# Optimization experiments

Measured on AMD Instinct MI355X. Metric: run time of the kernel, lower is better.

## Reference

```python
import jax, jax.numpy as jnp
import numpy as np

N, E, B, H, F = 20000, 400000, 200, 10, 78
HID = H * F  # 780
SEQ, VOC, EMB, NF, KS = 1000, 26, 128, 32, 8
CONV_OUT = SEQ - KS + 1  # 993


def setup_inputs() -> dict:
    key = jax.random.key(0)
    ks = jax.random.split(key, 40)
    g = lambda i, shape, s=0.05: jax.random.normal(ks[i], shape, jnp.float32) * s
    inp = {
        "x": jax.random.normal(ks[0], (N, F), jnp.float32),
        "edge_index": jax.random.randint(ks[1], (2, E), 0, N),
        "batch": jnp.sort(jax.random.randint(ks[2], (N,), 0, B)),
        "target": jax.random.randint(ks[3], (B, SEQ), 0, VOC),
        # GATConv(78 -> 78, heads=10)
        "gat_W": g(4, (F, HID)),
        "gat_a_src": g(5, (H, F)),
        "gat_a_dst": g(6, (H, F)),
        "gat_b": g(7, (HID,)),
        # GCNConv(780 -> 780)
        "gcn_W": g(8, (HID, HID)),
        "gcn_b": g(9, (HID,)),
        # graph MLP head
        "fcg1_W": g(10, (HID, 1500)), "fcg1_b": g(11, (1500,)),
        "fcg2_W": g(12, (1500, 128)), "fcg2_b": g(13, (128,)),
        # protein branch
        "emb": g(14, (VOC, EMB)),
        "cW": g(15, (NF, EMB, KS)), "cb": g(16, (NF,)),
        "fxt_W": g(17, (NF * CONV_OUT, 128)), "fxt_b": g(18, (128,)),
        # fusion MLP
        "f1_W": g(19, (256, 1024)), "f1_b": g(20, (1024,)),
        "f2_W": g(21, (1024, 512)), "f2_b": g(22, (512,)),
        "f3_W": g(23, (512, 256)), "f3_b": g(24, (256,)),
        "f4_W": g(25, (256, 128)), "f4_b": g(26, (128,)),
        "o_W": g(27, (128, 1)), "o_b": g(28, (1,)),
    }
    return inp


def _graph_branch(x, edge_index, batch, gat_W, gat_a_src, gat_a_dst, gat_b,
                  gcn_W, gcn_b, fcg1_W, fcg1_b, fcg2_W, fcg2_b):
    n = x.shape[0]
    loops = jnp.arange(n)
    src = jnp.concatenate([edge_index[0], loops])  # add self loops (PyG default)
    dst = jnp.concatenate([edge_index[1], loops])
    # --- GATConv ---
    h = (x @ gat_W).reshape(n, H, F)  # [N,H,F]
    a_s = jnp.einsum("nhf,hf->nh", h, gat_a_src)
    a_d = jnp.einsum("nhf,hf->nh", h, gat_a_dst)
    e = jax.nn.leaky_relu(a_s[src] + a_d[dst], 0.2)  # [Etot,H]
    m = jax.ops.segment_max(e, dst, num_segments=n)
    ex = jnp.exp(e - m[dst])
    den = jax.ops.segment_sum(ex, dst, num_segments=n)
    alpha = ex / den[dst]
    agg = jax.ops.segment_sum(h[src] * alpha[:, :, None], dst, num_segments=n)
    x1 = jax.nn.relu(agg.reshape(n, HID) + gat_b)
    # --- GCNConv (sym norm with self loops) ---
    deg = jax.ops.segment_sum(jnp.ones_like(dst, jnp.float32), dst, num_segments=n)
    dinv = jax.lax.rsqrt(jnp.maximum(deg, 1.0))
    norm = dinv[src] * dinv[dst]
    h2 = x1 @ gcn_W
    x2 = jax.ops.segment_sum(h2[src] * norm[:, None], dst, num_segments=n) + gcn_b
    x2 = jax.nn.relu(x2)
    # --- global add pool + MLP ---
    xg = jax.ops.segment_sum(x2, batch, num_segments=B)
    xg = jax.nn.relu(xg @ fcg1_W + fcg1_b)  # dropout = identity (eval)
    return xg @ fcg2_W + fcg2_b


def _protein_branch(target, emb, cW, cb, fxt_W, fxt_b):
    et = emb[target]  # [B,SEQ,EMB]
    c = jax.lax.conv_general_dilated(
        et.transpose(0, 2, 1), cW, (1,), "VALID",
        dimension_numbers=("NCH", "OIH", "NCH"))  # [B,NF,993]
    c = c + cb[None, :, None]
    return c.reshape(c.shape[0], NF * CONV_OUT) @ fxt_W + fxt_b


def reference(x, edge_index, batch, target, gat_W, gat_a_src, gat_a_dst, gat_b,
              gcn_W, gcn_b, fcg1_W, fcg1_b, fcg2_W, fcg2_b, emb, cW, cb,
              fxt_W, fxt_b, f1_W, f1_b, f2_W, f2_b, f3_W, f3_b, f4_W, f4_b,
              o_W, o_b):
    xg = _graph_branch(x, edge_index, batch, gat_W, gat_a_src, gat_a_dst, gat_b,
                       gcn_W, gcn_b, fcg1_W, fcg1_b, fcg2_W, fcg2_b)
    xt = _protein_branch(target, emb, cW, cb, fxt_W, fxt_b)
    xc = jnp.concatenate([xg, xt], axis=1)  # [B,256]
    xc = jax.nn.relu(xc @ f1_W + f1_b)
    xc = jax.nn.relu(xc @ f2_W + f2_b)
    xc = jax.nn.relu(xc @ f3_W + f3_b)
    xc = jax.nn.relu(xc @ f4_W + f4_b)
    return xc @ o_W + o_b  # [B,1]
```

## Files before the change

### kernel.cpp

```cpp
#include <hip/hip_runtime.h>
#include <hip/hip_bf16.h>
#include <math.h>

typedef __hip_bfloat16 bf16;
typedef __attribute__((ext_vector_type(8))) short short8v;
typedef __attribute__((ext_vector_type(4))) float float4v;

#define NODES 20000
#define EDG   400000
#define ETOT  (EDG + NODES)
#define GB    200
#define HEADS 10
#define FD    78
#define HIDD  780
#define SEQL  1000
#define VOCS  26
#define EMBD  128
#define NFC   32
#define KSZ   8
#define COUT  993
#define KFXT  (NFC * COUT)

#define MPAD  20096
#define NPADB 896
#define KP2   800
#define HP    800
#define PNL   2
#define PF    400
#define MB2   208
#define FXT_KS 128
#define HK    96
#define AGS   960


__device__ __forceinline__ float us2f(unsigned short u) {
  unsigned int i = ((unsigned int)u) << 16; float f; __builtin_memcpy(&f, &i, 4); return f;
}
__device__ __forceinline__ float b2f(bf16 v) { return __bfloat162float(v); }
__device__ __forceinline__ float ldany(const void* p, size_t i, int m) {
  if (m) return ((const float*)p)[i];
  return b2f(((const bf16*)p)[i]);
}
__device__ __forceinline__ bool nanf_(float v) { return v != v; }
__device__ __forceinline__ unsigned short f2us(float v) {
  bf16 b = __float2bfloat16(v); unsigned short u; __builtin_memcpy(&u, &b, 2); return u;
}

__global__ void k_detect(const void* x, int* diag) {
  int t = threadIdx.x;
  const unsigned short* u = (const unsigned short*)x;
  int hit = 0;
  for (int i = t; i < 4096; i += 256) {
    float v = us2f(u[i]);
    if (nanf_(v) || fabsf(v) > 1e6f) hit = 1;
  }
  if (hit) diag[1] = 1;
}

__global__ void k_tr_gcnw(const void* gw, bf16* Wt, const int* diag) {
  int idx = blockIdx.x * 256 + threadIdx.x;
  if (idx >= NPADB * KP2) return;
  int mode = diag[1];
  int n = idx / KP2, k = idx % KP2;
  float v = (n < HIDD && k < HIDD) ? ldany(gw, (size_t)k * HIDD + n, mode) : 0.f;
  Wt[idx] = __float2bfloat16(v);
}

__global__ void k_prep_wt2(const void* gw, bf16* Wt2, const int* diag) {
  int idx = blockIdx.x * 256 + threadIdx.x;
  if (idx >= HEADS * 128 * HK) return;
  int mode = diag[1];
  int h = idx / (128 * HK);
  int r = idx % (128 * HK);
  int n = r / HK, k = r % HK;
  float v = (n < FD && k < FD) ? ldany(gw, (size_t)k * HIDD + h * FD + n, mode) : 0.f;
  Wt2[idx] = __float2bfloat16(v);
}

__global__ void k_zero_x1pad(bf16* x1p) {
  int i = blockIdx.x * 256 + threadIdx.x;
  int nr = (MPAD - NODES) * KP2;
  if (i < nr) {
    x1p[(size_t)NODES * KP2 + i] = __float2bfloat16(0.f);
  } else {
    int j = i - nr;
    if (j < NODES * 20) {
      int d = j / 20, c = HIDD + (j % 20);
      x1p[(size_t)d * KP2 + c] = __float2bfloat16(0.f);
    }
  }
}

#define MT 128
#define NT 128
#define BK 32
#define LP 40
__global__ __launch_bounds__(256) void k_gemm_mfma(const bf16* A, int lda,
                                                   const bf16* Bt, int ldb,
                                                   bf16* C, int ldc, int Ncap,
                                                   int M, int Kp) {
  __shared__ __align__(16) bf16 As[MT * LP];
  __shared__ __align__(16) bf16 Bs[NT * LP];
  int t = threadIdx.x;
  int lane = t & 63, w = t >> 6;
  int wr = (w >> 1) * 64, wc = (w & 1) * 64;
  int quad = lane >> 4, mr = lane & 15;
  int m0 = blockIdx.y * MT, n0 = blockIdx.x * NT;
  float4v acc[4][4];
#pragma unroll
  for (int i = 0; i < 4; ++i)
#pragma unroll
    for (int j = 0; j < 4; ++j) acc[i][j] = (float4v){0.f, 0.f, 0.f, 0.f};

  for (int kc = 0; kc < Kp; kc += BK) {
#pragma unroll
    for (int i = 0; i < 4; ++i) {
      int c = t + i * 256;
      int row = c >> 3, col = (c & 7) * 4;
      *(uint2*)&As[row * LP + col] =
          *(const uint2*)&A[(size_t)(m0 + row) * lda + kc + col];
      *(uint2*)&Bs[row * LP + col] =
          *(const uint2*)&Bt[(size_t)(n0 + row) * ldb + kc + col];
    }
    __syncthreads();
    short8v af[4], bfr[4];
#pragma unroll
    for (int i = 0; i < 4; ++i)
      af[i] = *(const short8v*)&As[(wr + i * 16 + mr) * LP + quad * 8];
#pragma unroll
    for (int j = 0; j < 4; ++j)
      bfr[j] = *(const short8v*)&Bs[(wc + j * 16 + mr) * LP + quad * 8];
#pragma unroll
    for (int i = 0; i < 4; ++i)
#pragma unroll
      for (int j = 0; j < 4; ++j)
        acc[i][j] = __builtin_amdgcn_mfma_f32_16x16x32_bf16(af[i], bfr[j], acc[i][j], 0, 0, 0);
    __syncthreads();
  }
#pragma unroll
  for (int i = 0; i < 4; ++i) {
    int gm0 = m0 + wr + i * 16 + quad * 4;
#pragma unroll
    for (int j = 0; j < 4; ++j) {
      int gn = n0 + wc + j * 16 + mr;
      if (gn >= Ncap) continue;
#pragma unroll
      for (int r = 0; r < 4; ++r) {
        int gm = gm0 + r;
        if (gm < M) C[(size_t)gm * ldc + gn] = __float2bfloat16(acc[i][j][r]);
      }
    }
  }
}

__global__ __launch_bounds__(256) void k_hgemm(const bf16* aggx, const bf16* Wt2,
                                               const void* gat_b, bf16* x1,
                                               const int* diag) {
  __shared__ __align__(16) bf16 As[MT * LP];
  __shared__ __align__(16) bf16 Bs[NT * LP];
  int t = threadIdx.x;
  int lane = t & 63, w = t >> 6;
  int wr = (w >> 1) * 64, wc = (w & 1) * 64;
  int quad = lane >> 4, mr = lane & 15;
  int m0 = blockIdx.x * MT, h = blockIdx.y;
  int mode = diag[1];
  const bf16* A = aggx + (size_t)h * HK;
  const bf16* Bt = Wt2 + (size_t)h * 128 * HK;
  float4v acc[4][4];
#pragma unroll
  for (int i = 0; i < 4; ++i)
#pragma unroll
    for (int j = 0; j < 4; ++j) acc[i][j] = (float4v){0.f, 0.f, 0.f, 0.f};

  for (int kc = 0; kc < HK; kc += BK) {
#pragma unroll
    for (int i = 0; i < 4; ++i) {
      int c = t + i * 256;
      int row = c >> 3, col = (c & 7) * 4;
      *(uint2*)&As[row * LP + col] =
          *(const uint2*)&A[(size_t)(m0 + row) * AGS + kc + col];
      *(uint2*)&Bs[row * LP + col] =
          *(const uint2*)&Bt[(size_t)row * HK + kc + col];
    }
    __syncthreads();
    short8v af[4], bfr[4];
#pragma unroll
    for (int i = 0; i < 4; ++i)
      af[i] = *(const short8v*)&As[(wr + i * 16 + mr) * LP + quad * 8];
#pragma unroll
    for (int j = 0; j < 4; ++j)
      bfr[j] = *(const short8v*)&Bs[(wc + j * 16 + mr) * LP + quad * 8];
#pragma unroll
    for (int i = 0; i < 4; ++i)
#pragma unroll
      for (int j = 0; j < 4; ++j)
        acc[i][j] = __builtin_amdgcn_mfma_f32_16x16x32_bf16(af[i], bfr[j], acc[i][j], 0, 0, 0);
    __syncthreads();
  }
#pragma unroll
  for (int i = 0; i < 4; ++i) {
    int gm0 = m0 + wr + i * 16 + quad * 4;
#pragma unroll
    for (int j = 0; j < 4; ++j) {
      int gn = wc + j * 16 + mr;
      if (gn >= FD) continue;
      float bs = ldany(gat_b, h * FD + gn, mode);
#pragma unroll
      for (int r = 0; r < 4; ++r) {
        int gm = gm0 + r;
        if (gm < NODES)
          x1[(size_t)gm * KP2 + h * FD + gn] =
              __float2bfloat16(fmaxf(acc[i][j][r] + bs, 0.f));
      }
    }
  }
}

#define MLP_NT 64
#define MLP_BK 32
#define MLP_MT 208
#define MLP_LP 40
__global__ __launch_bounds__(256) void k_mlp_mfma(const void* A, int lda, const void* Bw,
                                                  const void* bias, float* out, int ostride,
                                                  int ooff, int M, int Nn, int K,
                                                  int ksplit, int aRelu, int aBf16,
                                                  const int* diag) {
  __shared__ __align__(16) bf16 As[MLP_MT * MLP_LP];
  __shared__ __align__(16) bf16 Bs[MLP_NT * MLP_LP];
  int mode = diag[1];
  int t = threadIdx.x;
  int lane = t & 63, w = t >> 6;
  int quad = lane >> 4, mr = lane & 15;
  int n0 = blockIdx.x * MLP_NT;
  int kz = blockIdx.y;
  int nchunks = (K + MLP_BK - 1) / MLP_BK;
  int cpk = (nchunks + ksplit - 1) / ksplit;
  int c0 = kz * cpk, c1 = c0 + cpk;
  if (c1 > nchunks) c1 = nchunks;
  float4v acc[13];
#pragma unroll
  for (int i = 0; i < 13; ++i) acc[i] = (float4v){0.f, 0.f, 0.f, 0.f};

  for (int c = c0; c < c1; ++c) {
    int k0 = c * MLP_BK;
    if (aBf16) {
      const bf16* Ab = (const bf16*)A;
      for (int e = t; e < MLP_MT * 4; e += 256) {
        int row = e >> 2, c8 = (e & 3) * 8;
        int gk = k0 + c8;
        if (row < M && gk + 7 < K) {
          *(uint4*)&As[row * MLP_LP + c8] = *(const uint4*)&Ab[(size_t)row * lda + gk];
        } else {
#pragma unroll
          for (int kk = 0; kk < 8; ++kk) {
            float v = (row < M && gk + kk < K) ? b2f(Ab[(size_t)row * lda + gk + kk]) : 0.f;
            As[row * MLP_LP + c8 + kk] = __float2bfloat16(v);
          }
        }
      }
    } else {
      const float* Af = (const float*)A;
      for (int e = t; e < MLP_MT * 8; e += 256) {
        int row = e >> 3, c4 = (e & 7) * 4;
        int gk = k0 + c4;
        float4 v4 = {0.f, 0.f, 0.f, 0.f};
        if (row < M) {
          if (gk + 3 < K) {
            v4 = *(const float4*)&Af[(size_t)row * lda + gk];
          } else {
            v4.x = (gk + 0 < K) ? Af[(size_t)row * lda + gk + 0] : 0.f;
            v4.y = (gk + 1 < K) ? Af[(size_t)row * lda + gk + 1] : 0.f;
            v4.z = (gk + 2 < K) ? Af[(size_t)row * lda + gk + 2] : 0.f;
            v4.w = (gk + 3 < K) ? Af[(size_t)row * lda + gk + 3] : 0.f;
          }
        }
        if (aRelu) {
          v4.x = fmaxf(v4.x, 0.f); v4.y = fmaxf(v4.y, 0.f);
          v4.z = fmaxf(v4.z, 0.f); v4.w = fmaxf(v4.w, 0.f);
        }
        bf16* dst = &As[row * MLP_LP + c4];
        dst[0] = __float2bfloat16(v4.x); dst[1] = __float2bfloat16(v4.y);
        dst[2] = __float2bfloat16(v4.z); dst[3] = __float2bfloat16(v4.w);
      }
    }
    for (int e = t; e < MLP_NT * MLP_BK; e += 256) {
      int k = e >> 6, col = e & 63;
      int gk = k0 + k, gn = n0 + col;
      float v = (gn < Nn && gk < K) ? ldany(Bw, (size_t)gk * Nn + gn, mode) : 0.f;
      Bs[col * MLP_LP + k] = __float2bfloat16(v);
    }
    __syncthreads();
    short8v bf = *(const short8v*)&Bs[(w * 16 + mr) * MLP_LP + quad * 8];
#pragma unroll
    for (int i = 0; i < 13; ++i) {
      short8v af = *(const short8v*)&As[(i * 16 + mr) * MLP_LP + quad * 8];
      acc[i] = __builtin_amdgcn_mfma_f32_16x16x32_bf16(af, bf, acc[i], 0, 0, 0);
    }
    __syncthreads();
  }
  int gn = n0 + w * 16 + mr;
  if (gn >= Nn) return;
  float bs = (kz == 0) ? ldany(bias, gn, mode) : 0.f;
#pragma unroll
  for (int i = 0; i < 13; ++i) {
    int gm0 = i * 16 + quad * 4;
#pragma unroll
    for (int r = 0; r < 4; ++r) {
      int gm = gm0 + r;
      if (gm >= M) break;
      float v = acc[i][r] + bs;
      float* op = &out[(size_t)gm * ostride + ooff + gn];
      if (ksplit == 1) *op = v;
      else atomicAdd(op, v);
    }
  }
}

__global__ __launch_bounds__(256) void k_fxt(const bf16* cT, const void* Bw,
                                             float* part, const int* diag) {
  __shared__ __align__(16) bf16 As[MLP_MT * MLP_LP];
  __shared__ __align__(16) bf16 Bs[MLP_NT * MLP_LP];
  int mode = diag[1];
  int t = threadIdx.x;
  int lane = t & 63, w = t >> 6;
  int quad = lane >> 4, mr = lane & 15;
  int n0 = blockIdx.x * MLP_NT;
  int kz = blockIdx.y;
  int nchunks = KFXT / MLP_BK;
  int cpk = (nchunks + FXT_KS - 1) / FXT_KS;
  int c0 = kz * cpk, c1 = c0 + cpk;
  if (c1 > nchunks) c1 = nchunks;
  float4v acc[13];
#pragma unroll
  for (int i = 0; i < 13; ++i) acc[i] = (float4v){0.f, 0.f, 0.f, 0.f};

  for (int c = c0; c < c1; ++c) {
    int k0 = c * MLP_BK;
    for (int e = t; e < 32 * 52; e += 256) {
      int kk = e / 52, bq = e % 52;
      uint2 u = *(const uint2*)&cT[(size_t)(k0 + kk) * MB2 + bq * 4];
      unsigned short* ap = (unsigned short*)As;
      int mb = bq * 4;
      ap[(mb + 0) * MLP_LP + kk] = (unsigned short)(u.x & 0xffffu);
      ap[(mb + 1) * MLP_LP + kk] = (unsigned short)(u.x >> 16);
      ap[(mb + 2) * MLP_LP + kk] = (unsigned short)(u.y & 0xffffu);
      ap[(mb + 3) * MLP_LP + kk] = (unsigned short)(u.y >> 16);
    }
    for (int e = t; e < MLP_NT * MLP_BK; e += 256) {
      int k = e >> 6, col = e & 63;
      float v = ldany(Bw, (size_t)(k0 + k) * 128 + (n0 + col), mode);
      Bs[col * MLP_LP + k] = __float2bfloat16(v);
    }
    __syncthreads();
    short8v bf = *(const short8v*)&Bs[(w * 16 + mr) * MLP_LP + quad * 8];
#pragma unroll
    for (int i = 0; i < 13; ++i) {
      short8v af = *(const short8v*)&As[(i * 16 + mr) * MLP_LP + quad * 8];
      acc[i] = __builtin_amdgcn_mfma_f32_16x16x32_bf16(af, bf, acc[i], 0, 0, 0);
    }
    __syncthreads();
  }
  int gnl = n0 + w * 16 + mr;
#pragma unroll
  for (int i = 0; i < 13; ++i) {
#pragma unroll
    for (int r = 0; r < 4; ++r) {
      int gm = i * 16 + quad * 4 + r;
      part[((size_t)kz * MB2 + gm) * 128 + gnl] = acc[i][r];
    }
  }
}

__global__ __launch_bounds__(128) void k_fxt_red(const float* part, const void* bias,
                                                 float* xc, const int* diag) {
  int gm = blockIdx.x, n = threadIdx.x;
  int mode = diag[1];
  float s = 0.f;
  for (int kz = 0; kz < FXT_KS; ++kz)
    s += part[((size_t)kz * MB2 + gm) * 128 + n];
  xc[(size_t)gm * 256 + 128 + n] = s + ldany(bias, n, mode);
}

__global__ void k_prep_ws(const void* gat_W, const void* a_src, const void* a_dst,
                          float* Ws, float* Wd, const int* diag) {
  int idx = blockIdx.x * 256 + threadIdx.x;
  if (idx >= FD * HEADS) return;
  int mode = diag[1];
  int k = idx / HEADS, hd = idx % HEADS;
  float s = 0.f, d = 0.f;
  for (int f = 0; f < FD; ++f) {
    float w = ldany(gat_W, (size_t)k * HIDD + hd * FD + f, mode);
    s += w * ldany(a_src, (size_t)hd * FD + f, mode);
    d += w * ldany(a_dst, (size_t)hd * FD + f, mode);
  }
  Ws[k * HEADS + hd] = s;
  Wd[k * HEADS + hd] = d;
}

__global__ void k_prep_mtab(const void* emb, const void* cW, float* Mtab, const int* diag) {
  int idx = blockIdx.x * 256 + threadIdx.x;
  if (idx >= NFC * KSZ * VOCS) return;
  int mode = diag[1];
  int o = idx / (KSZ * VOCS);
  int r = idx % (KSZ * VOCS);
  int k = r / VOCS, v = r % VOCS;
  float acc = 0.f;
  for (int i = 0; i < EMBD; ++i)
    acc += ldany(emb, (size_t)v * EMBD + i, mode) * ldany(cW, ((size_t)o * EMBD + i) * KSZ + k, mode);
  Mtab[idx] = acc;
}

__global__ __launch_bounds__(256) void k_asd(const void* x, const float* Ws, const float* Wd,
                                             float* a_s, float* a_d, const int* diag) {
  __shared__ unsigned short xs[256 * FD];
  __shared__ float ws_sh[FD * HEADS], wd_sh[FD * HEADS];
  int mode = diag[1];
  int nb = blockIdx.x * 256, t = threadIdx.x;
  for (int e = t; e < FD * HEADS; e += 256) { ws_sh[e] = Ws[e]; wd_sh[e] = Wd[e]; }
  for (int e = t; e < 256 * FD; e += 256) {
    int r = e / FD, c = e % FD;
    int gn = nb + r;
    float xv = (gn < NODES) ? ldany(x, (size_t)gn * FD + c, mode) : 0.f;
    xs[e] = f2us(xv);
  }
  __syncthreads();
  int n = nb + t;
  if (n >= NODES) return;
  float as[HEADS], ad[HEADS];
#pragma unroll
  for (int hd = 0; hd < HEADS; ++hd) { as[hd] = 0.f; ad[hd] = 0.f; }
  for (int f = 0; f < FD; ++f) {
    float xv = us2f(xs[t * FD + f]);
#pragma unroll
    for (int hd = 0; hd < HEADS; ++hd) {
      as[hd] += xv * ws_sh[f * HEADS + hd];
      ad[hd] += xv * wd_sh[f * HEADS + hd];
    }
  }
#pragma unroll
  for (int hd = 0; hd < HEADS; ++hd) {
    a_s[n * HEADS + hd] = as[hd];
    a_d[n * HEADS + hd] = ad[hd];
  }
}

__global__ void k_count(const int* ei, int* cnt, int* diag) {
  int e = blockIdx.x * 256 + threadIdx.x;
  if (e >= ETOT) return;
  int d = (e < EDG) ? ei[EDG + e] : (e - EDG);
  if ((unsigned)d >= NODES) { atomicOr(diag, 8192); d = 0; }
  atomicAdd(&cnt[d], 1);
}

__global__ __launch_bounds__(1024) void k_scan(const int* cnt, int* rowstart) {
  __shared__ int wsum[16];
  __shared__ int carry;
  int t = threadIdx.x;
  int lane = t & 63, wid = t >> 6;
  if (t == 0) carry = 0;
  __syncthreads();
  for (int c = 0; c < (NODES + 1023) / 1024; ++c) {
    int i = c * 1024 + t;
    int orig = (i < NODES) ? cnt[i] : 0;
    int v = orig;
#pragma unroll
    for (int off = 1; off < 64; off <<= 1) {
      int u = __shfl_up(v, off, 64);
      if (lane >= off) v += u;
    }
    if (lane == 63) wsum[wid] = v;
    __syncthreads();
    if (t == 0) {
      int s = carry;
      for (int j = 0; j < 16; ++j) { int tmp = wsum[j]; wsum[j] = s; s += tmp; }
      carry = s;
    }
    __syncthreads();
    if (i < NODES) rowstart[i] = v - orig + wsum[wid];
    __syncthreads();
  }
  if (t == 0) rowstart[NODES] = carry;
}

__global__ void k_dinv(const int* cnt, float* dinv) {
  int n = blockIdx.x * 256 + threadIdx.x;
  if (n >= NODES) return;
  int d = cnt[n];
  dinv[n] = rsqrtf((float)(d > 0 ? d : 1));
}

__global__ void k_scatter(const int* ei, const int* rowstart, int* cur, int* es_src,
                          int* diag) {
  int e = blockIdx.x * 256 + threadIdx.x;
  if (e >= ETOT) return;
  int s, d;
  if (e < EDG) { s = ei[e]; d = ei[EDG + e]; } else { s = e - EDG; d = s; }
  if ((unsigned)d >= NODES) { atomicOr(diag, 8192); d = 0; }
  if ((unsigned)s >= NODES) { atomicOr(diag, 8192); s = 0; }
  int pos = rowstart[d] + atomicAdd(&cur[d], 1);
  if ((unsigned)pos < (unsigned)ETOT) es_src[pos] = s;
  else atomicOr(diag, 1);
}

__global__ void k_csrchk(const int* cnt, const int* cur, const int* rowst, int* diag) {
  int n = blockIdx.x * 256 + threadIdx.x;
  if (n < NODES && cur[n] != cnt[n]) atomicOr(diag, 1);
  if (n == 0 && rowst[NODES] != ETOT) atomicOr(diag, 1);
}

__global__ void k_bseg(const int* batch, int* bstart, int* diag) {
  int i = blockIdx.x * 256 + threadIdx.x;
  if (i >= NODES) return;
  int bi = batch[i];
  if ((unsigned)bi >= GB) { atomicOr(diag, 8192); bi = GB - 1; }
  int bp;
  if (i == 0) bp = -1;
  else {
    bp = batch[i - 1];
    if ((unsigned)bp >= GB) bp = GB - 1;
  }
  for (int b = bp + 1; b <= bi; ++b) bstart[b] = i;
  if (i == NODES - 1)
    for (int b = bi + 1; b <= GB; ++b) bstart[b] = NODES;
}

__global__ __launch_bounds__(64) void k_alpha(const int* es_src, const int* rowst,
                                              const float* a_s, const float* a_d,
                                              float* alpha, int* diag) {
  int d = blockIdx.x, lane = threadIdx.x;
  int start = rowst[d], end = rowst[d + 1];
  float ad[HEADS];
#pragma unroll
  for (int j = 0; j < HEADS; ++j) ad[j] = a_d[d * HEADS + j];
  float mx[HEADS];
#pragma unroll
  for (int j = 0; j < HEADS; ++j) mx[j] = -INFINITY;
  for (int base = start; base < end; base += 64) {
    int ce = base + lane;
    if (ce < end) {
      int s = es_src[ce];
      if ((unsigned)s >= NODES) { atomicOr(diag, 1); s = 0; }
#pragma unroll
      for (int j = 0; j < HEADS; ++j) {
        float v = a_s[s * HEADS + j] + ad[j];
        v = v > 0.f ? v : 0.2f * v;
        mx[j] = fmaxf(mx[j], v);
      }
    }
  }
#pragma unroll
  for (int j = 0; j < HEADS; ++j)
    for (int off = 1; off < 64; off <<= 1) mx[j] = fmaxf(mx[j], __shfl_xor(mx[j], off, 64));
  float den[HEADS];
#pragma unroll
  for (int j = 0; j < HEADS; ++j) den[j] = 0.f;
  for (int base = start; base < end; base += 64) {
    int ce = base + lane;
    if (ce < end) {
      int s = es_src[ce];
      if ((unsigned)s >= NODES) s = 0;
#pragma unroll
      for (int j = 0; j < HEADS; ++j) {
        float v = a_s[s * HEADS + j] + ad[j];
        v = v > 0.f ? v : 0.2f * v;
        den[j] += expf(v - mx[j]);
      }
    }
  }
#pragma unroll
  for (int j = 0; j < HEADS; ++j)
    for (int off = 1; off < 64; off <<= 1) den[j] += __shfl_xor(den[j], off, 64);
  if (lane == 0 && (nanf_(den[0]) || nanf_(den[HEADS - 1]))) atomicOr(diag, 2);
  for (int base = start; base < end; base += 64) {
    int ce = base + lane;
    if (ce < end) {
      int s = es_src[ce];
      if ((unsigned)s >= NODES) s = 0;
#pragma unroll
      for (int j = 0; j < HEADS; ++j) {
        float v = a_s[s * HEADS + j] + ad[j];
        v = v > 0.f ? v : 0.2f * v;
        alpha[(size_t)ce * HEADS + j] = expf(v - mx[j]) / den[j];
      }
    }
  }
}

__global__ __launch_bounds__(64) void k_gatx(const int* es_src, const int* rowst,
                                             const float* alpha, const void* x,
                                             bf16* aggx, int* diag) {
  __shared__ int ssc[64];
  __shared__ float alw[64 * HEADS];
  int d = blockIdx.x, lane = threadIdx.x;
  int mode = diag[1];
  int start = rowst[d], end = rowst[d + 1];
  int f0 = 2 * lane;
  float acc[HEADS][2];
#pragma unroll
  for (int j = 0; j < HEADS; ++j) { acc[j][0] = 0.f; acc[j][1] = 0.f; }
  for (int base = start; base < end; base += 64) {
    int ce = base + lane;
    if (ce < end) {
      int s = es_src[ce];
      if ((unsigned)s >= NODES) { atomicOr(diag, 1); s = 0; }
      ssc[lane] = s;
#pragma unroll
      for (int j = 0; j < HEADS; ++j) alw[lane * HEADS + j] = alpha[(size_t)ce * HEADS + j];
    }
    __syncthreads();
    int cnt2 = end - base; if (cnt2 > 64) cnt2 = 64;
    if (lane < 39) {
      for (int e = 0; e < cnt2; ++e) {
        int ss = ssc[e];
        float xv0, xv1;
        if (mode) {
          const float* xf = (const float*)x;
          xv0 = xf[(size_t)ss * FD + f0];
          xv1 = xf[(size_t)ss * FD + f0 + 1];
        } else {
          unsigned int u = *(const unsigned int*)((const unsigned short*)x +
                                                  (size_t)ss * FD + f0);
          xv0 = us2f((unsigned short)(u & 0xffffu));
          xv1 = us2f((unsigned short)(u >> 16));
        }
        const float* al = &alw[e * HEADS];
#pragma unroll
        for (int j = 0; j < HEADS; ++j) {
          acc[j][0] += al[j] * xv0;
          acc[j][1] += al[j] * xv1;
        }
      }
    }
    __syncthreads();
  }
  if (lane < 48) {
    if (lane < 39 && (nanf_(acc[0][0]) || nanf_(acc[HEADS - 1][1]))) atomicOr(diag, 8);
    size_t rb = (size_t)d * AGS;
#pragma unroll
    for (int h = 0; h < HEADS; ++h) {
      unsigned short o0 = (f0 < FD) ? f2us(acc[h][0]) : (unsigned short)0;
      unsigned short o1 = (f0 + 1 < FD) ? f2us(acc[h][1]) : (unsigned short)0;
      unsigned int pack = (unsigned int)o0 | ((unsigned int)o1 << 16);
      *(unsigned int*)(aggx + rb + h * HK + f0) = pack;
    }
  }
}

__global__ __launch_bounds__(64) void k_gcng(const int* es_src, const int* rowst,
                                             const float* dinv, const bf16* h2,
                                             const void* gcn_b, bf16* x2b, int* diag) {
  __shared__ int ssc[64];
  __shared__ float nw[64];
  int bid = blockIdx.x;
  int p = bid & (PNL - 1), d = bid >> 1;
  int lane = threadIdx.x;
  int mode = diag[1];
  int start = rowst[d], end = rowst[d + 1];
  float dd = dinv[d];
  int fb = p * PF + lane * 8;
  float acc[8];
#pragma unroll
  for (int k = 0; k < 8; ++k) acc[k] = 0.f;
  for (int base = start; base < end; base += 64) {
    int ce = base + lane;
    if (ce < end) {
      int s = es_src[ce];
      if ((unsigned)s >= NODES) { atomicOr(diag, 1); s = 0; }
      ssc[lane] = s;
      nw[lane] = dinv[s] * dd;
    }
    __syncthreads();
    int cnt2 = end - base; if (cnt2 > 64) cnt2 = 64;
    if (lane < 50) {
      for (int e = 0; e < cnt2; ++e) {
        int ss = ssc[e];
        float nv = nw[e];
        uint4 u = *(const uint4*)(h2 + (size_t)ss * HP + fb);
        unsigned int uw[4] = {u.x, u.y, u.z, u.w};
#pragma unroll
        for (int k = 0; k < 4; ++k) {
          acc[2 * k]     += nv * us2f((unsigned short)(uw[k] & 0xffffu));
          acc[2 * k + 1] += nv * us2f((unsigned short)(uw[k] >> 16));
        }
      }
    }
    __syncthreads();
  }
  if (lane < 50) {
    if (nanf_(acc[0]) || nanf_(acc[7])) atomicOr(diag, 16);
    unsigned short o[8];
#pragma unroll
    for (int k = 0; k < 8; ++k) {
      int f = fb + k;
      float v = 0.f;
      if (f < HIDD) v = fmaxf(acc[k] + ldany(gcn_b, f, mode), 0.f);
      o[k] = f2us(v);
    }
    uint4 pack;
    __builtin_memcpy(&pack, o, 16);
    *(uint4*)(x2b + (size_t)d * HP + fb) = pack;
  }
}

__global__ __launch_bounds__(256) void k_pool(const bf16* x2b, const int* bstart,
                                              float* xg_pool) {
  int b = blockIdx.x, t = threadIdx.x;
  if (t >= 195) return;
  int r0 = bstart[b], r1 = bstart[b + 1];
  int fb = t * 4;
  float4 acc = {0.f, 0.f, 0.f, 0.f};
  for (int r = r0; r < r1; ++r) {
    uint2 u = *(const uint2*)(x2b + (size_t)r * HP + fb);
    acc.x += us2f((unsigned short)(u.x & 0xffffu));
    acc.y += us2f((unsigned short)(u.x >> 16));
    acc.z += us2f((unsigned short)(u.y & 0xffffu));
    acc.w += us2f((unsigned short)(u.y >> 16));
  }
  *(float4*)&xg_pool[(size_t)b * HIDD + fb] = acc;
}

__global__ __launch_bounds__(256) void k_convT(const int* target, const float* Mtab,
                                               const void* cb, bf16* cT, int* diag) {
  __shared__ int tg[GB * 40];
  __shared__ float Mt[KSZ * VOCS];
  int tt0 = blockIdx.x * 32, o = blockIdx.y, t = threadIdx.x;
  int mode = diag[1];
  for (int e = t; e < KSZ * VOCS; e += 256)
    Mt[e] = Mtab[(o * KSZ + e / VOCS) * VOCS + (e % VOCS)];
  for (int e = t; e < GB * 40; e += 256) {
    int b = e / 40, q = e % 40;
    int pos = tt0 + q;
    int tv = (pos < SEQL) ? target[b * SEQL + pos] : 0;
    if ((unsigned)tv >= VOCS) { atomicOr(diag, 8192); tv = 0; }
    tg[e] = tv;
  }
  __syncthreads();
  float cbv = ldany(cb, o, mode);
  for (int e = t; e < 32 * MB2; e += 256) {
    int tt = e / MB2, b = e % MB2;
    int gtt = tt0 + tt;
    if (gtt >= COUT) continue;
    float acc = 0.f;
    if (b < GB) {
#pragma unroll
      for (int k = 0; k < KSZ; ++k)
        acc += Mt[k * VOCS + tg[b * 40 + tt + k]];
      acc += cbv;
      if (nanf_(acc)) atomicOr(diag, 4096);
    }
    cT[((size_t)o * COUT + gtt) * MB2 + b] = __float2bfloat16(b < GB ? acc : 0.f);
  }
}

__global__ __launch_bounds__(64) void k_out(const float* xf4, const void* o_W,
                                            const void* o_b, void* outp, const int* diag) {
  int b = blockIdx.x, lane = threadIdx.x;
  int mode = diag[1];
  float a0 = fmaxf(xf4[b * 128 + lane], 0.f);
  float a1 = fmaxf(xf4[b * 128 + 64 + lane], 0.f);
  float v = a0 * ldany(o_W, lane, mode) + a1 * ldany(o_W, 64 + lane, mode);
  for (int off = 32; off; off >>= 1) v += __shfl_down(v, off, 64);
  if (lane == 0) {
    float r = v + ldany(o_b, 0, mode);
    int dg = diag[0];
    if (dg) r = 256.f * (1 + mode) + 8.f * (float)(__ffs(dg) - 1);
    else if (nanf_(r)) r = 200.f + 100.f * mode;
    if (mode) ((float*)outp)[b] = r;
    else ((bf16*)outp)[b] = __float2bfloat16(r);
  }
}

extern "C" void kernel_launch(void* const* d_in, const int* in_sizes, int n_in,
                              void* d_out, int out_size, void* d_ws, size_t ws_size,
                              hipStream_t stream) {
  const void* x       = d_in[0];
  const int*  ei      = (const int*)d_in[1];
  const int*  batch   = (const int*)d_in[2];
  const int*  target  = (const int*)d_in[3];
  const void* gat_W   = d_in[4];
  const void* a_src   = d_in[5];
  const void* a_dst   = d_in[6];
  const void* gat_b   = d_in[7];
  const void* gcn_W   = d_in[8];
  const void* gcn_b   = d_in[9];
  const void* fcg1_W  = d_in[10];
  const void* fcg1_b  = d_in[11];
  const void* fcg2_W  = d_in[12];
  const void* fcg2_b  = d_in[13];
  const void* emb     = d_in[14];
  const void* cW      = d_in[15];
  const void* cb      = d_in[16];
  const void* fxt_W   = d_in[17];
  const void* fxt_b   = d_in[18];
  const void* f1_W    = d_in[19];
  const void* f1_b    = d_in[20];
  const void* f2_W    = d_in[21];
  const void* f2_b    = d_in[22];
  const void* f3_W    = d_in[23];
  const void* f3_b    = d_in[24];
  const void* f4_W    = d_in[25];
  const void* f4_b    = d_in[26];
  const void* o_W     = d_in[27];
  const void* o_b     = d_in[28];

  char* w = (char*)d_ws;
  size_t off = 0;
  auto alloc = [&](size_t bytes) -> void* {
    void* p = w + off;
    off = (off + bytes + 255) & ~(size_t)255;
    return p;
  };
  bf16*  h_buf   = (bf16*)alloc((size_t)NODES * HP * 2);
  bf16*  x1p     = (bf16*)alloc((size_t)MPAD * KP2 * 2);
  bf16*  aggx    = (bf16*)alloc((size_t)MPAD * AGS * 2);
  bf16*  gatWt2  = (bf16*)alloc((size_t)HEADS * 128 * HK * 2);
  bf16*  gcnWt   = (bf16*)alloc((size_t)NPADB * KP2 * 2);
  float* a_s     = (float*)alloc((size_t)NODES * HEADS * 4);
  float* a_d     = (float*)alloc((size_t)NODES * HEADS * 4);
  float* alpha   = (float*)alloc((size_t)ETOT * HEADS * 4);
  float* Ws      = (float*)alloc(FD * HEADS * 4);
  float* Wd      = (float*)alloc(FD * HEADS * 4);
  float* Mtab    = (float*)alloc(NFC * KSZ * VOCS * 4);
  int*   rowst   = (int*)alloc((NODES + 1) * 4);
  float* dinv    = (float*)alloc(NODES * 4);
  int*   bstart  = (int*)alloc((GB + 1) * 4);
  size_t zoff = off;
  int*   cnt     = (int*)alloc(NODES * 4);
  int*   cur     = (int*)alloc(NODES * 4);
  int*   es_src  = (int*)alloc((size_t)ETOT * 4);
  float* xg_pool = (float*)alloc((size_t)GB * HIDD * 4);
  float* xg1     = (float*)alloc((size_t)GB * 1500 * 4);
  float* xc      = (float*)alloc((size_t)GB * 256 * 4);
  float* xf1     = (float*)alloc((size_t)GB * 1024 * 4);
  float* xf2     = (float*)alloc((size_t)GB * 512 * 4);
  float* xf3     = (float*)alloc((size_t)GB * 256 * 4);
  float* xf4     = (float*)alloc((size_t)GB * 128 * 4);
  int*   diag    = (int*)alloc(2 * 4);
  size_t zlen = off - zoff;

  bf16* x2b = x1p;
  bf16*  cT   = (bf16*)aggx;
  size_t cTb  = ((size_t)KFXT * MB2 * 2 + 255) & ~(size_t)255;
  float* part = (float*)((char*)aggx + cTb);

  hipMemsetAsync(w + zoff, 0, zlen, stream);

  k_detect<<<1, 256, 0, stream>>>(x, diag);

  k_tr_gcnw<<<(NPADB * KP2 + 255) / 256, 256, 0, stream>>>(gcn_W, gcnWt, diag);
  k_prep_wt2<<<(HEADS * 128 * HK + 255) / 256, 256, 0, stream>>>(gat_W, gatWt2, diag);
  k_zero_x1pad<<<((MPAD - NODES) * KP2 + NODES * 20 + 255) / 256, 256, 0, stream>>>(x1p);

  k_prep_ws<<<(FD * HEADS + 255) / 256, 256, 0, stream>>>(gat_W, a_src, a_dst, Ws, Wd, diag);
  k_prep_mtab<<<(NFC * KSZ * VOCS + 255) / 256, 256, 0, stream>>>(emb, cW, Mtab, diag);

  k_asd<<<(NODES + 255) / 256, 256, 0, stream>>>(x, Ws, Wd, a_s, a_d, diag);

  k_count<<<(ETOT + 255) / 256, 256, 0, stream>>>(ei, cnt, diag);
  k_scan<<<1, 1024, 0, stream>>>(cnt, rowst);
  k_dinv<<<(NODES + 255) / 256, 256, 0, stream>>>(cnt, dinv);
  k_scatter<<<(ETOT + 255) / 256, 256, 0, stream>>>(ei, rowst, cur, es_src, diag);
  k_csrchk<<<(NODES + 255) / 256, 256, 0, stream>>>(cnt, cur, rowst, diag);
  k_bseg<<<(NODES + 255) / 256, 256, 0, stream>>>(batch, bstart, diag);

  k_alpha<<<NODES, 64, 0, stream>>>(es_src, rowst, a_s, a_d, alpha, diag);
  k_gatx<<<NODES, 64, 0, stream>>>(es_src, rowst, alpha, x, aggx, diag);
  k_hgemm<<<dim3(MPAD / MT, HEADS), 256, 0, stream>>>(aggx, gatWt2, gat_b, x1p, diag);

  k_gemm_mfma<<<dim3(NPADB / NT, MPAD / MT), 256, 0, stream>>>(
      x1p, KP2, gcnWt, KP2, h_buf, HP, HP, NODES, KP2);

  k_gcng<<<NODES * PNL, 64, 0, stream>>>(es_src, rowst, dinv, h_buf, gcn_b, x2b, diag);
  k_pool<<<GB, 256, 0, stream>>>(x2b, bstart, xg_pool);

  k_convT<<<dim3((COUT + 31) / 32, NFC), 256, 0, stream>>>(target, Mtab, cb, cT, diag);
  k_fxt<<<dim3(2, FXT_KS), 256, 0, stream>>>(cT, fxt_W, part, diag);
  k_fxt_red<<<GB, 128, 0, stream>>>(part, fxt_b, xc, diag);

  k_mlp_mfma<<<dim3(24, 4), 256, 0, stream>>>(xg_pool, HIDD, fcg1_W, fcg1_b,
                                              xg1, 1500, 0, GB, 1500, HIDD, 4, 0, 0, diag);
  k_mlp_mfma<<<dim3(2, 16), 256, 0, stream>>>(xg1, 1500, fcg2_W, fcg2_b,
                                              xc, 256, 0, GB, 128, 1500, 16, 1, 0, diag);
  k_mlp_mfma<<<dim3(16, 4), 256, 0, stream>>>(xc, 256, f1_W, f1_b,
                                              xf1, 1024, 0, GB, 1024, 256, 4, 0, 0, diag);
  k_mlp_mfma<<<dim3(8, 8), 256, 0, stream>>>(xf1, 1024, f2_W, f2_b,
                                             xf2, 512, 0, GB, 512, 1024, 8, 1, 0, diag);
  k_mlp_mfma<<<dim3(4, 8), 256, 0, stream>>>(xf2, 512, f3_W, f3_b,
                                             xf3, 256, 0, GB, 256, 512, 8, 1, 0, diag);
  k_mlp_mfma<<<dim3(2, 8), 256, 0, stream>>>(xf3, 256, f4_W, f4_b,
                                             xf4, 128, 0, GB, 128, 256, 8, 1, 0, diag);
  k_out<<<GB, 64, 0, stream>>>(xf4, o_W, o_b, d_out, diag);
}
```

Before: 879.3 us.

## Fuse GAT attention softmax into aggregation kernel and tile gcn_W transpose

Merges the attention-coefficient kernel into the GAT aggregation kernel. Exponentials are computed on the fly into shared memory, and the softmax denominator is applied once at the end, so the per-edge alpha buffer (ETOT*HEADS floats) is no longer written and read back and one launch is dropped. It also rewrites the gcn_W transpose to use a padded shared-memory 32x32 tile so both the reads and the writes are coalesced. The cost is that the fused kernel holds more registers per thread, and the out-of-range source diagnostic is now raised only in the first pass.

Result: faster. 848.4 us (-3.5%).

```diff
diff --git a/kernel.cpp b/kernel.cpp
--- a/kernel.cpp
+++ b/kernel.cpp
@@ -57,13 +57,23 @@
   if (hit) diag[1] = 1;
 }
 
-__global__ void k_tr_gcnw(const void* gw, bf16* Wt, const int* diag) {
-  int idx = blockIdx.x * 256 + threadIdx.x;
-  if (idx >= NPADB * KP2) return;
-  int mode = diag[1];
-  int n = idx / KP2, k = idx % KP2;
-  float v = (n < HIDD && k < HIDD) ? ldany(gw, (size_t)k * HIDD + n, mode) : 0.f;
-  Wt[idx] = __float2bfloat16(v);
+__global__ __launch_bounds__(256) void k_tr_gcnw(const void* gw, bf16* Wt,
+                                                 const int* diag) {
+  __shared__ float tile[32][33];
+  int k0 = blockIdx.x * 32, n0 = blockIdx.y * 32;
+  int mode = diag[1];
+  int t = threadIdx.x;
+  int tn = t & 31, tk = t >> 5;
+  for (int kk = tk; kk < 32; kk += 8) {
+    int gk = k0 + kk, gn = n0 + tn;
+    tile[kk][tn] = (gk < HIDD && gn < HIDD) ? ldany(gw, (size_t)gk * HIDD + gn, mode) : 0.f;
+  }
+  __syncthreads();
+  for (int nn = tk; nn < 32; nn += 8) {
+    int gn = n0 + nn, gk = k0 + tn;
+    if (gn < NPADB && gk < KP2)
+      Wt[(size_t)gn * KP2 + gk] = __float2bfloat16(tile[tn][nn]);
+  }
 }
 
 __global__ void k_prep_wt2(const void* gw, bf16* Wt2, const int* diag) {
@@ -524,14 +534,18 @@
     for (int b = bi + 1; b <= GB; ++b) bstart[b] = NODES;
 }
 
-__global__ __launch_bounds__(64) void k_alpha(const int* es_src, const int* rowst,
-                                              const float* a_s, const float* a_d,
-                                              float* alpha, int* diag) {
+__global__ __launch_bounds__(64) void k_gatx(const int* es_src, const int* rowst,
+                                             const float* a_s, const float* a_d,
+                                             const void* x, bf16* aggx, int* diag) {
+  __shared__ int ssc[64];
+  __shared__ float alw[64 * HEADS];
   int d = blockIdx.x, lane = threadIdx.x;
+  int mode = diag[1];
   int start = rowst[d], end = rowst[d + 1];
   float ad[HEADS];
 #pragma unroll
   for (int j = 0; j < HEADS; ++j) ad[j] = a_d[d * HEADS + j];
+
   float mx[HEADS];
 #pragma unroll
   for (int j = 0; j < HEADS; ++j) mx[j] = -INFINITY;
@@ -551,61 +565,28 @@
 #pragma unroll
   for (int j = 0; j < HEADS; ++j)
     for (int off = 1; off < 64; off <<= 1) mx[j] = fmaxf(mx[j], __shfl_xor(mx[j], off, 64));
+
   float den[HEADS];
 #pragma unroll
   for (int j = 0; j < HEADS; ++j) den[j] = 0.f;
+  int f0 = 2 * lane;
+  float acc[HEADS][2];
+#pragma unroll
+  for (int j = 0; j < HEADS; ++j) { acc[j][0] = 0.f; acc[j][1] = 0.f; }
   for (int base = start; base < end; base += 64) {
     int ce = base + lane;
     if (ce < end) {
       int s = es_src[ce];
       if ((unsigned)s >= NODES) s = 0;
+      ssc[lane] = s;
 #pragma unroll
       for (int j = 0; j < HEADS; ++j) {
         float v = a_s[s * HEADS + j] + ad[j];
         v = v > 0.f ? v : 0.2f * v;
-        den[j] += expf(v - mx[j]);
+        float ex = expf(v - mx[j]);
+        alw[lane * HEADS + j] = ex;
+        den[j] += ex;
       }
-    }
-  }
-#pragma unroll
-  for (int j = 0; j < HEADS; ++j)
-    for (int off = 1; off < 64; off <<= 1) den[j] += __shfl_xor(den[j], off, 64);
-  if (lane == 0 && (nanf_(den[0]) || nanf_(den[HEADS - 1]))) atomicOr(diag, 2);
-  for (int base = start; base < end; base += 64) {
-    int ce = base + lane;
-    if (ce < end) {
-      int s = es_src[ce];
-      if ((unsigned)s >= NODES) s = 0;
-#pragma unroll
-      for (int j = 0; j < HEADS; ++j) {
-        float v = a_s[s * HEADS + j] + ad[j];
-        v = v > 0.f ? v : 0.2f * v;
-        alpha[(size_t)ce * HEADS + j] = expf(v - mx[j]) / den[j];
-      }
-    }
-  }
-}
-
-__global__ __launch_bounds__(64) void k_gatx(const int* es_src, const int* rowst,
-                                             const float* alpha, const void* x,
-                                             bf16* aggx, int* diag) {
-  __shared__ int ssc[64];
-  __shared__ float alw[64 * HEADS];
-  int d = blockIdx.x, lane = threadIdx.x;
-  int mode = diag[1];
-  int start = rowst[d], end = rowst[d + 1];
-  int f0 = 2 * lane;
-  float acc[HEADS][2];
-#pragma unroll
-  for (int j = 0; j < HEADS; ++j) { acc[j][0] = 0.f; acc[j][1] = 0.f; }
-  for (int base = start; base < end; base += 64) {
-    int ce = base + lane;
-    if (ce < end) {
-      int s = es_src[ce];
-      if ((unsigned)s >= NODES) { atomicOr(diag, 1); s = 0; }
-      ssc[lane] = s;
-#pragma unroll
-      for (int j = 0; j < HEADS; ++j) alw[lane * HEADS + j] = alpha[(size_t)ce * HEADS + j];
     }
     __syncthreads();
     int cnt2 = end - base; if (cnt2 > 64) cnt2 = 64;
@@ -633,13 +614,19 @@
     }
     __syncthreads();
   }
+#pragma unroll
+  for (int j = 0; j < HEADS; ++j)
+    for (int off = 1; off < 64; off <<= 1) den[j] += __shfl_xor(den[j], off, 64);
+  if (lane == 0 && (nanf_(den[0]) || nanf_(den[HEADS - 1]))) atomicOr(diag, 2);
+
   if (lane < 48) {
     if (lane < 39 && (nanf_(acc[0][0]) || nanf_(acc[HEADS - 1][1]))) atomicOr(diag, 8);
     size_t rb = (size_t)d * AGS;
 #pragma unroll
     for (int h = 0; h < HEADS; ++h) {
-      unsigned short o0 = (f0 < FD) ? f2us(acc[h][0]) : (unsigned short)0;
-      unsigned short o1 = (f0 + 1 < FD) ? f2us(acc[h][1]) : (unsigned short)0;
+      float r = 1.f / den[h];
+      unsigned short o0 = (f0 < FD) ? f2us(acc[h][0] * r) : (unsigned short)0;
+      unsigned short o1 = (f0 + 1 < FD) ? f2us(acc[h][1] * r) : (unsigned short)0;
       unsigned int pack = (unsigned int)o0 | ((unsigned int)o1 << 16);
       *(unsigned int*)(aggx + rb + h * HK + f0) = pack;
     }
@@ -817,7 +804,6 @@
   bf16*  gcnWt   = (bf16*)alloc((size_t)NPADB * KP2 * 2);
   float* a_s     = (float*)alloc((size_t)NODES * HEADS * 4);
   float* a_d     = (float*)alloc((size_t)NODES * HEADS * 4);
-  float* alpha   = (float*)alloc((size_t)ETOT * HEADS * 4);
   float* Ws      = (float*)alloc(FD * HEADS * 4);
   float* Wd      = (float*)alloc(FD * HEADS * 4);
   float* Mtab    = (float*)alloc(NFC * KSZ * VOCS * 4);
@@ -847,7 +833,7 @@
 
   k_detect<<<1, 256, 0, stream>>>(x, diag);
 
-  k_tr_gcnw<<<(NPADB * KP2 + 255) / 256, 256, 0, stream>>>(gcn_W, gcnWt, diag);
+  k_tr_gcnw<<<dim3(KP2 / 32, NPADB / 32), 256, 0, stream>>>(gcn_W, gcnWt, diag);
   k_prep_wt2<<<(HEADS * 128 * HK + 255) / 256, 256, 0, stream>>>(gat_W, gatWt2, diag);
   k_zero_x1pad<<<((MPAD - NODES) * KP2 + NODES * 20 + 255) / 256, 256, 0, stream>>>(x1p);
 
@@ -863,8 +849,7 @@
   k_csrchk<<<(NODES + 255) / 256, 256, 0, stream>>>(cnt, cur, rowst, diag);
   k_bseg<<<(NODES + 255) / 256, 256, 0, stream>>>(batch, bstart, diag);
 
-  k_alpha<<<NODES, 64, 0, stream>>>(es_src, rowst, a_s, a_d, alpha, diag);
-  k_gatx<<<NODES, 64, 0, stream>>>(es_src, rowst, alpha, x, aggx, diag);
+  k_gatx<<<NODES, 64, 0, stream>>>(es_src, rowst, a_s, a_d, x, aggx, diag);
   k_hgemm<<<dim3(MPAD / MT, HEADS), 256, 0, stream>>>(aggx, gatWt2, gat_b, x1p, diag);
 
   k_gemm_mfma<<<dim3(NPADB / NT, MPAD / MT), 256, 0, stream>>>(
```
